# Kernel tuning notes

Measured on AMD Instinct MI355X. Metric: run time of the kernel, lower is better.

## Reference

```python
import jax, jax.numpy as jnp
import numpy as np

HEADS = 16  # module init arg `heads`


def setup_inputs() -> dict:
    key = jax.random.key(0)
    k1, k2, k3 = jax.random.split(key, 3)
    B, T, D = 2, 2048, 1024
    x = jax.random.normal(k1, (B, T, D), dtype=jnp.float32)
    w_qkv = jax.random.normal(k2, (D, 3 * D), dtype=jnp.float32) * (1.0 / np.sqrt(D))
    w_proj = jax.random.normal(k3, (D, D), dtype=jnp.float32) * (1.0 / np.sqrt(D))
    b_proj = jnp.zeros((D,), dtype=jnp.float32)
    return {"x": x, "w_qkv": w_qkv, "w_proj": w_proj, "b_proj": b_proj,
            "window": 16, "stride": 16}


def reference(x, w_qkv, w_proj, b_proj, window, stride):
    B, T, D = x.shape
    H = HEADS
    hd = D // H
    scale = 1.0 / np.sqrt(hd)

    qkv = x @ w_qkv                              # [B,T,3D]
    qkv = qkv.reshape(B, T, 3, H, hd)
    q = jnp.transpose(qkv[:, :, 0], (0, 2, 1, 3))  # [B,H,T,hd]
    k = jnp.transpose(qkv[:, :, 1], (0, 2, 1, 3))
    v = jnp.transpose(qkv[:, :, 2], (0, 2, 1, 3))

    # Local window attention: pad front with zeros (matches F.pad), gather
    # sliding windows so patches[..., t, w, :] = k_padded[..., t + w, :].
    pad = window - 1
    k_pad = jnp.pad(k, ((0, 0), (0, 0), (pad, 0), (0, 0)))
    v_pad = jnp.pad(v, ((0, 0), (0, 0), (pad, 0), (0, 0)))
    win_idx = jnp.arange(T)[:, None] + jnp.arange(window)[None, :]  # [T,W]
    pk = k_pad[:, :, win_idx]                    # [B,H,T,W,hd]
    pv = v_pad[:, :, win_idx]                    # [B,H,T,W,hd]

    attn_local = jnp.einsum('bhtd,bhtwd->bhtw', q, pk) * scale
    attn_local = jax.nn.softmax(attn_local, axis=-1)  # zero-pad keys included, as in torch
    out_local = jnp.einsum('bhtw,bhtwd->bhtd', attn_local, pv)

    # Strided global attention
    g_idx = jnp.arange(0, T, stride)
    kg = k[:, :, g_idx]                          # [B,H,G,hd]
    vg = v[:, :, g_idx]
    attn_g = jnp.einsum('bhtd,bhgd->bhtg', q, kg) * scale
    attn_g = jax.nn.softmax(attn_g, axis=-1)
    out_global = jnp.einsum('bhtg,bhgd->bhtd', attn_g, vg)

    out = out_local + out_global                 # [B,H,T,hd]
    out = jnp.transpose(out, (0, 2, 1, 3)).reshape(B, T, D)
    return out @ w_proj + b_proj
```

## Files before the change

kernel.cpp:

```cpp
#include <hip/hip_runtime.h>
#include <hip/hip_bf16.h>

#define BB 2
#define TT 2048
#define DD 1024
#define HH 16
#define HD 64
#define WIN 16
#define NG 128
#define QKVLD 3072
#define QB 128

typedef __bf16 bf16x8 __attribute__((ext_vector_type(8)));
typedef _Float16 f16x8 __attribute__((ext_vector_type(8)));
typedef float f32x4 __attribute__((ext_vector_type(4)));
typedef _Float16 h2 __attribute__((ext_vector_type(2)));
typedef __fp16 pk2_t __attribute__((ext_vector_type(2)));

__device__ __forceinline__ unsigned short f2bf(float f) {
    union { float f; unsigned int i; } x; x.f = f;
    unsigned int r = x.i + 0x7FFFu + ((x.i >> 16) & 1u);
    return (unsigned short)(r >> 16);
}
__device__ __forceinline__ unsigned short f2h(float f) {
    union { _Float16 h; unsigned short u; } x; x.h = (_Float16)f; return x.u;
}
__device__ __forceinline__ unsigned int pk2h(float lo, float hi) {
    union { pk2_t h; unsigned int u; } X;
    X.h = __builtin_amdgcn_cvt_pkrtz(lo, hi);
    return X.u;
}

__device__ __forceinline__ void gll16(const unsigned short* g, unsigned short* l) {
    __builtin_amdgcn_global_load_lds(
        (const __attribute__((address_space(1))) void*)g,
        (__attribute__((address_space(3))) void*)l,
        16, 0, 0);
}

__global__ __launch_bounds__(256) void prepass_kernel(
    const float* __restrict__ x,
    const float* __restrict__ w_qkv,
    const float* __restrict__ w_proj,
    unsigned short* __restrict__ xb,
    unsigned short* __restrict__ wqkvT,
    unsigned short* __restrict__ wprojT)
{
    __shared__ float tile[64][65];
    const int bid = blockIdx.x;
    const int tid = threadIdx.x;

    if (bid < 2048) {
        const size_t i = ((size_t)bid * 256 + tid) * 8;
        float4 f0 = *(const float4*)(x + i);
        float4 f1 = *(const float4*)(x + i + 4);
        ushort4 a = { f2bf(f0.x), f2bf(f0.y), f2bf(f0.z), f2bf(f0.w) };
        ushort4 b = { f2bf(f1.x), f2bf(f1.y), f2bf(f1.z), f2bf(f1.w) };
        *(ushort4*)(xb + i) = a;
        *(ushort4*)(xb + i + 4) = b;
        return;
    }

    const float* w;
    unsigned short* wT;
    int nblk, kblk, N;
    if (bid < 2816) {
        const int b2 = bid - 2048;
        w = w_qkv; wT = wqkvT; N = 3072;
        nblk = b2 % 48; kblk = b2 / 48;
    } else {
        const int b2 = bid - 2816;
        w = w_proj; wT = wprojT; N = 1024;
        nblk = b2 % 16; kblk = b2 / 16;
    }
    const int K = 1024;
    const int n0 = nblk * 64, k0 = kblk * 64;

    {
        const int krow = tid >> 2;
        const int nc0  = (tid & 3) * 16;
        const float* src = w + (size_t)(k0 + krow) * N + n0 + nc0;
        float4 f0 = *(const float4*)(src);
        float4 f1 = *(const float4*)(src + 4);
        float4 f2 = *(const float4*)(src + 8);
        float4 f3 = *(const float4*)(src + 12);
        *(float4*)&tile[krow][nc0]      = f0;
        *(float4*)&tile[krow][nc0 + 4]  = f1;
        *(float4*)&tile[krow][nc0 + 8]  = f2;
        *(float4*)&tile[krow][nc0 + 12] = f3;
    }
    __syncthreads();
    #pragma unroll
    for (int rep = 0; rep < 2; ++rep) {
        const int n   = (tid >> 3) + rep * 32;
        const int kc0 = (tid & 7) * 8;
        union { uint4 v; unsigned short u[8]; } o;
        #pragma unroll
        for (int j = 0; j < 8; ++j) o.u[j] = f2bf(tile[kc0 + j][n]);
        *(uint4*)(wT + (size_t)(n0 + n) * K + k0 + kc0) = o.v;
    }
}

template<int MODE, int TN>
__global__ __launch_bounds__(256) void gemm_kernel(
    const unsigned short* __restrict__ A,
    const unsigned short* __restrict__ Bt,
    void* __restrict__ Cp,
    const float* __restrict__ bias,
    int M, int N, int K)
{
    constexpr int NJ = TN / 32;
    constexpr int BRW = TN / 4;
    __shared__ __align__(16) unsigned short As[128 * 64];
    __shared__ __align__(16) unsigned short Bs[TN * 64];
    const int tid  = threadIdx.x;
    const int wave = tid >> 6;
    const int lane = tid & 63;
    const int lm   = lane & 15;
    const int quad = lane >> 4;
    const int wm   = (wave >> 1) * 64;
    const int wn   = (wave & 1) * (TN / 2);
    const int bm   = blockIdx.y * 128;
    const int bn   = blockIdx.x * TN;

    f32x4 acc[4][NJ];
    const f32x4 z4 = { 0.f, 0.f, 0.f, 0.f };
    #pragma unroll
    for (int i = 0; i < 4; ++i)
        #pragma unroll
        for (int j = 0; j < NJ; ++j) acc[i][j] = z4;

    const int lrow = lane >> 3;
    const int lcol = ((lane & 7) ^ lrow) * 8;
    const unsigned short* gA = A  + (size_t)(bm + wave * 32  + lrow) * K + lcol;
    const unsigned short* gB = Bt + (size_t)(bn + wave * BRW + lrow) * K + lcol;
    unsigned short* lA = &As[(wave * 32)  * 64];
    unsigned short* lB = &Bs[(wave * BRW) * 64];

    const int sx = lm & 7;
    for (int k0 = 0; k0 < K; k0 += 64) {
        __syncthreads();
        #pragma unroll
        for (int s = 0; s < 4; ++s)
            gll16(gA + k0 + (size_t)(8 * s) * K, lA + (8 * s) * 64);
        #pragma unroll
        for (int s = 0; s < BRW / 8; ++s)
            gll16(gB + k0 + (size_t)(8 * s) * K, lB + (8 * s) * 64);
        __syncthreads();
        #pragma unroll
        for (int kk = 0; kk < 2; ++kk) {
            bf16x8 af[4], bfr[NJ];
            #pragma unroll
            for (int i = 0; i < 4; ++i)
                af[i] = *(const bf16x8*)&As[(wm + i * 16 + lm) * 64
                                            + (((kk * 4 + quad) ^ sx) * 8)];
            #pragma unroll
            for (int j = 0; j < NJ; ++j)
                bfr[j] = *(const bf16x8*)&Bs[(wn + j * 16 + lm) * 64
                                             + (((kk * 4 + quad) ^ sx) * 8)];
            #pragma unroll
            for (int i = 0; i < 4; ++i)
                #pragma unroll
                for (int j = 0; j < NJ; ++j)
                    acc[i][j] = __builtin_amdgcn_mfma_f32_16x16x32_bf16(
                        af[i], bfr[j], acc[i][j], 0, 0, 0);
        }
    }

    #pragma unroll
    for (int i = 0; i < 4; ++i) {
        #pragma unroll
        for (int r = 0; r < 4; ++r) {
            const int row = bm + wm + i * 16 + quad * 4 + r;
            #pragma unroll
            for (int j = 0; j < NJ; ++j) {
                const int col = bn + wn + j * 16 + lm;
                float v = acc[i][j][r];
                if constexpr (MODE == 0) {
                    ((unsigned short*)Cp)[(size_t)row * N + col] = f2h(v);
                } else {
                    ((float*)Cp)[(size_t)row * N + col] = v + bias[col];
                }
            }
        }
    }
}

__device__ __forceinline__ f16x8 pfrag(unsigned int fa0, unsigned int fa1,
                                       unsigned int fb0, unsigned int fb1,
                                       int quad) {
    const unsigned int t16_0 = (quad == 2) ? fb0 : fa0;
    const unsigned int t16_1 = (quad == 2) ? fb1 : fa1;
    const unsigned int t32_0 = (quad == 0) ? fb0 : fa0;
    const unsigned int t32_1 = (quad == 0) ? fb1 : fa1;
    const unsigned int t48_0 = (quad == 1) ? fb0 : fa0;
    const unsigned int t48_1 = (quad == 1) ? fb1 : fa1;
    const unsigned int s16_0 = (unsigned int)__shfl_xor((int)t16_0, 16, 64);
    const unsigned int s16_1 = (unsigned int)__shfl_xor((int)t16_1, 16, 64);
    const unsigned int s32_0 = (unsigned int)__shfl_xor((int)t32_0, 32, 64);
    const unsigned int s32_1 = (unsigned int)__shfl_xor((int)t32_1, 32, 64);
    const unsigned int s48_0 = (unsigned int)__shfl_xor((int)t48_0, 48, 64);
    const unsigned int s48_1 = (unsigned int)__shfl_xor((int)t48_1, 48, 64);
    unsigned int w0, w1, w2, w3;
    if (quad == 0)      { w0 = fa0;   w1 = fa1;   w2 = s16_0; w3 = s16_1; }
    else if (quad == 1) { w0 = s48_0; w1 = s48_1; w2 = s32_0; w3 = s32_1; }
    else if (quad == 2) { w0 = s32_0; w1 = s32_1; w2 = s48_0; w3 = s48_1; }
    else                { w0 = s16_0; w1 = s16_1; w2 = fb0;   w3 = fb1;   }
    union { unsigned int u[4]; f16x8 v; } R;
    R.u[0] = w0; R.u[1] = w1; R.u[2] = w2; R.u[3] = w3;
    return R.v;
}

__global__ __launch_bounds__(512, 4) void attn_kernel(
    const unsigned short* __restrict__ qkv,
    unsigned short* __restrict__ attn_out)
{
    __shared__ __align__(16) unsigned short smem[19584];
    unsigned short* const Kg  = smem;
    unsigned short* const Kl  = smem + 9216;
    unsigned short* const VgT = smem;
    unsigned short* const VlT = smem + 9216;
    unsigned short* const Ep  = smem;

    const int tid  = threadIdx.x;
    const int wave = tid >> 6;
    const int lane = tid & 63;
    const int lm   = lane & 15;
    const int quad = lane >> 4;
    const int bx   = blockIdx.x;
    const int bh   = bx >> 4;
    const int t0   = (bx & 15) * QB;
    const int b    = bh >> 4;
    const int h    = bh & 15;

    const size_t baseQ = (size_t)(b * TT) * QKVLD + h * HD;

    const int r  = (tid & 255) >> 1;
    const int hf = tid & 1;
    uint4 va[4];
    if (tid < 256) {
        const unsigned short* ks = qkv + baseQ + 1024 + (size_t)(16 * r) * QKVLD + hf * 32;
        const unsigned short* vs = ks + 1024;
        unsigned short* kd = Kg + r * 72 + hf * 32;
        #pragma unroll
        for (int j = 0; j < 4; ++j) *(uint4*)(kd + j * 8) = *(const uint4*)(ks + j * 8);
        #pragma unroll
        for (int j = 0; j < 4; ++j) va[j] = *(const uint4*)(vs + j * 8);
    } else {
        const int tl = t0 - 15 + r;
        unsigned short* kld = Kl + r * 72 + hf * 32;
        if (tl < 0 || tl >= TT) {
            const uint4 z = { 0, 0, 0, 0 };
            #pragma unroll
            for (int j = 0; j < 4; ++j) { *(uint4*)(kld + j * 8) = z; va[j] = z; }
        } else {
            const unsigned short* kls = qkv + baseQ + 1024 + (size_t)tl * QKVLD + hf * 32;
            const unsigned short* vls = kls + 1024;
            #pragma unroll
            for (int j = 0; j < 4; ++j) *(uint4*)(kld + j * 8) = *(const uint4*)(kls + j * 8);
            #pragma unroll
            for (int j = 0; j < 4; ++j) va[j] = *(const uint4*)(vls + j * 8);
        }
    }
    if (tid < 32) {
        const int r2 = 128 + (tid >> 1);
        const int tl = t0 - 15 + r2;
        unsigned short* kld = Kl + r2 * 72 + hf * 32;
        if (tl < 0 || tl >= TT) {
            const uint4 z = { 0, 0, 0, 0 };
            #pragma unroll
            for (int j = 0; j < 4; ++j) *(uint4*)(kld + j * 8) = z;
        } else {
            const unsigned short* kls = qkv + baseQ + 1024 + (size_t)tl * QKVLD + hf * 32;
            #pragma unroll
            for (int j = 0; j < 4; ++j) *(uint4*)(kld + j * 8) = *(const uint4*)(kls + j * 8);
        }
    }

    f16x8 qf[2];
    {
        const unsigned short* qrow = qkv + baseQ + (size_t)(t0 + 16 * wave + lm) * QKVLD;
        const h2 sc = { (_Float16)0.125f, (_Float16)0.125f };
        #pragma unroll
        for (int c = 0; c < 2; ++c) {
            union { uint4 u; h2 hh[4]; f16x8 v; } U;
            U.u = *(const uint4*)(qrow + c * 32 + quad * 8);
            #pragma unroll
            for (int k = 0; k < 4; ++k) U.hh[k] *= sc;
            qf[c] = U.v;
        }
    }

    __syncthreads();

    f32x4 sg[8], sl[2];
    const f32x4 z4 = { 0.f, 0.f, 0.f, 0.f };
    #pragma unroll
    for (int f = 0; f < 8; ++f) sg[f] = z4;
    sl[0] = z4; sl[1] = z4;
    __builtin_amdgcn_s_setprio(1);
    #pragma unroll
    for (int f = 0; f < 8; ++f)
        #pragma unroll
        for (int c = 0; c < 2; ++c)
            sg[f] = __builtin_amdgcn_mfma_f32_16x16x32_f16(
                *(const f16x8*)&Kg[(16 * f + lm) * 72 + c * 32 + quad * 8], qf[c],
                sg[f], 0, 0, 0);
    #pragma unroll
    for (int f = 0; f < 2; ++f)
        #pragma unroll
        for (int c = 0; c < 2; ++c)
            sl[f] = __builtin_amdgcn_mfma_f32_16x16x32_f16(
                *(const f16x8*)&Kl[(16 * wave + 16 * f + lm) * 72 + c * 32 + quad * 8], qf[c],
                sl[f], 0, 0, 0);
    __builtin_amdgcn_s_setprio(0);

    float invg, invl;
    {
        float dg = 0.f, dl = 0.f;
        #pragma unroll
        for (int f = 0; f < 8; ++f)
            #pragma unroll
            for (int rr = 0; rr < 4; ++rr) {
                float e = __expf(sg[f][rr]); sg[f][rr] = e; dg += e;
            }
        #pragma unroll
        for (int f = 0; f < 2; ++f)
            #pragma unroll
            for (int rr = 0; rr < 4; ++rr) {
                const int j2 = 16 * f + quad * 4 + rr;
                const bool in = (j2 >= lm) && (j2 <= lm + 15);
                float e = in ? __expf(sl[f][rr]) : 0.f;
                sl[f][rr] = e; dl += e;
            }
        dg += __shfl_xor(dg, 16, 64);
        dg += __shfl_xor(dg, 32, 64);
        dl += __shfl_xor(dl, 16, 64);
        dl += __shfl_xor(dl, 32, 64);
        invg = 1.f / dg;
        invl = 1.f / dl;
    }

    f16x8 pa0, pa1, pa2, pa3, pal;
    {
        #pragma unroll
        for (int f = 0; f < 8; ++f)
            #pragma unroll
            for (int rr = 0; rr < 4; ++rr) sg[f][rr] *= invg;
        #pragma unroll
        for (int f = 0; f < 2; ++f)
            #pragma unroll
            for (int rr = 0; rr < 4; ++rr) sl[f][rr] *= invl;
        pa0 = pfrag(pk2h(sg[0][0], sg[0][1]), pk2h(sg[0][2], sg[0][3]),
                    pk2h(sg[1][0], sg[1][1]), pk2h(sg[1][2], sg[1][3]), quad);
        pa1 = pfrag(pk2h(sg[2][0], sg[2][1]), pk2h(sg[2][2], sg[2][3]),
                    pk2h(sg[3][0], sg[3][1]), pk2h(sg[3][2], sg[3][3]), quad);
        pa2 = pfrag(pk2h(sg[4][0], sg[4][1]), pk2h(sg[4][2], sg[4][3]),
                    pk2h(sg[5][0], sg[5][1]), pk2h(sg[5][2], sg[5][3]), quad);
        pa3 = pfrag(pk2h(sg[6][0], sg[6][1]), pk2h(sg[6][2], sg[6][3]),
                    pk2h(sg[7][0], sg[7][1]), pk2h(sg[7][2], sg[7][3]), quad);
        pal = pfrag(pk2h(sl[0][0], sl[0][1]), pk2h(sl[0][2], sl[0][3]),
                    pk2h(sl[1][0], sl[1][1]), pk2h(sl[1][2], sl[1][3]), quad);
    }

    __syncthreads();

    {
        union { uint4 u[4]; unsigned short s[32]; } U;
        #pragma unroll
        for (int j = 0; j < 4; ++j) U.u[j] = va[j];
        if (tid < 256) {
            #pragma unroll
            for (int j = 0; j < 32; ++j) VgT[(hf * 32 + j) * 136 + r] = U.s[j];
        } else {
            #pragma unroll
            for (int j = 0; j < 32; ++j) VlT[(hf * 32 + j) * 152 + r] = U.s[j];
        }
        if (tid < 32) {
            const int r2 = 128 + (tid >> 1);
            const int tl = t0 - 15 + r2;
            union { uint4 u[4]; unsigned short s[32]; } W;
            if (tl < 0 || tl >= TT) {
                const uint4 z = { 0, 0, 0, 0 };
                #pragma unroll
                for (int j = 0; j < 4; ++j) W.u[j] = z;
            } else {
                const unsigned short* vls = qkv + baseQ + 2048 + (size_t)tl * QKVLD + hf * 32;
                #pragma unroll
                for (int j = 0; j < 4; ++j) W.u[j] = *(const uint4*)(vls + j * 8);
            }
            #pragma unroll
            for (int j = 0; j < 32; ++j) VlT[(hf * 32 + j) * 152 + r2] = W.s[j];
        }
    }

    __syncthreads();

    f32x4 o[4];
    #pragma unroll
    for (int c = 0; c < 4; ++c) o[c] = z4;
    __builtin_amdgcn_s_setprio(1);
    #pragma unroll
    for (int c = 0; c < 4; ++c) {
        o[c] = __builtin_amdgcn_mfma_f32_16x16x32_f16(
            pa0, *(const f16x8*)&VgT[(16 * c + lm) * 136 + 0 * 32 + quad * 8], o[c], 0, 0, 0);
        o[c] = __builtin_amdgcn_mfma_f32_16x16x32_f16(
            pa1, *(const f16x8*)&VgT[(16 * c + lm) * 136 + 1 * 32 + quad * 8], o[c], 0, 0, 0);
        o[c] = __builtin_amdgcn_mfma_f32_16x16x32_f16(
            pa2, *(const f16x8*)&VgT[(16 * c + lm) * 136 + 2 * 32 + quad * 8], o[c], 0, 0, 0);
        o[c] = __builtin_amdgcn_mfma_f32_16x16x32_f16(
            pa3, *(const f16x8*)&VgT[(16 * c + lm) * 136 + 3 * 32 + quad * 8], o[c], 0, 0, 0);
        o[c] = __builtin_amdgcn_mfma_f32_16x16x32_f16(
            pal, *(const f16x8*)&VlT[(16 * c + lm) * 152 + 16 * wave + quad * 8], o[c], 0, 0, 0);
    }
    __builtin_amdgcn_s_setprio(0);

    __syncthreads();

    {
        unsigned short* const Pw = Ep + wave * (16 * 72);
        #pragma unroll
        for (int rr = 0; rr < 4; ++rr) {
            unsigned short* orow_p = Pw + (quad * 4 + rr) * 72;
            #pragma unroll
            for (int c = 0; c < 4; ++c) orow_p[16 * c + lm] = f2bf(o[c][rr]);
        }
        const int orow = lane >> 2;
        const int ocol = (lane & 3) * 16;
        const uint4 d0 = *(const uint4*)&Pw[orow * 72 + ocol];
        const uint4 d1 = *(const uint4*)&Pw[orow * 72 + ocol + 8];
        unsigned short* dst = attn_out + (size_t)(b * TT + t0 + 16 * wave + orow) * DD + h * HD + ocol;
        *(uint4*)(dst)     = d0;
        *(uint4*)(dst + 8) = d1;
    }
}

extern "C" void kernel_launch(void* const* d_in, const int* in_sizes, int n_in,
                              void* d_out, int out_size, void* d_ws, size_t ws_size,
                              hipStream_t stream) {
    const float* x      = (const float*)d_in[0];
    const float* w_qkv  = (const float*)d_in[1];
    const float* w_proj = (const float*)d_in[2];
    const float* b_proj = (const float*)d_in[3];

    char* ws = (char*)d_ws;
    unsigned short* qkv    = (unsigned short*)ws;
    unsigned short* xb     = (unsigned short*)(ws + 25165824);
    unsigned short* attnb  = xb;
    unsigned short* wqkvT  = (unsigned short*)(ws + 25165824 + 8388608);
    unsigned short* wprojT = (unsigned short*)(ws + 25165824 + 8388608 + 6291456);
    float* out = (float*)d_out;

    prepass_kernel<<<3072, 256, 0, stream>>>(x, w_qkv, w_proj, xb, wqkvT, wprojT);

    gemm_kernel<0, 128><<<dim3(3072 / 128, 4096 / 128), 256, 0, stream>>>(
        xb, wqkvT, qkv, nullptr, 4096, 3072, 1024);

    attn_kernel<<<dim3(BB * HH * (TT / QB)), 512, 0, stream>>>(qkv, attnb);

    gemm_kernel<1, 64><<<dim3(1024 / 64, 4096 / 128), 256, 0, stream>>>(
        attnb, wprojT, out, b_proj, 4096, 1024, 1024);
}
```

Measured before the change: 150.4 us.

## Add 256x192 double-buffered GEMM kernel for QKV projection

Replaces the 128x128-tile QKV GEMM with a new 512-thread kernel that uses 256x192 output tiles, a double-buffered K loop of 32 with global-to-LDS async loads, and XOR-swizzled LDS layout. Larger tiles raise arithmetic intensity and operand reuse per block, and the double buffering overlaps loads with MFMA work. The grid shrinks to 256 blocks, roughly one per CU, so tail effects and occupancy may limit the gain. The epilogue writes fp16 scalars without vectorization.

```diff
diff --git a/kernel.cpp b/kernel.cpp
--- a/kernel.cpp
+++ b/kernel.cpp
@@ -98,6 +98,83 @@
         #pragma unroll
         for (int j = 0; j < 8; ++j) o.u[j] = f2bf(tile[kc0 + j][n]);
         *(uint4*)(wT + (size_t)(n0 + n) * K + k0 + kc0) = o.v;
+    }
+}
+
+__global__ __launch_bounds__(512, 2) void gemm_big_kernel(
+    const unsigned short* __restrict__ A,
+    const unsigned short* __restrict__ Bt,
+    unsigned short* __restrict__ C)
+{
+    __shared__ __align__(16) unsigned short As[2][256 * 32];
+    __shared__ __align__(16) unsigned short Bs[2][192 * 32];
+    const int tid  = threadIdx.x;
+    const int wave = tid >> 6;
+    const int lane = tid & 63;
+    const int lm   = lane & 15;
+    const int quad = lane >> 4;
+    const int wm   = (wave >> 1) * 64;
+    const int wn   = (wave & 1) * 96;
+    const int bm   = blockIdx.y * 256;
+    const int bn   = blockIdx.x * 192;
+    const int K = 1024, N = 3072;
+
+    f32x4 acc[4][6];
+    const f32x4 z4 = { 0.f, 0.f, 0.f, 0.f };
+    #pragma unroll
+    for (int i = 0; i < 4; ++i)
+        #pragma unroll
+        for (int j = 0; j < 6; ++j) acc[i][j] = z4;
+
+    const int srow = lane >> 2;
+    const int schk = (lane & 3) ^ (srow & 3);
+    const unsigned short* gA0 = A  + (size_t)(bm + (2 * wave)     * 16 + srow) * K + schk * 8;
+    const unsigned short* gA1 = A  + (size_t)(bm + (2 * wave + 1) * 16 + srow) * K + schk * 8;
+    const unsigned short* gB0 = Bt + (size_t)(bn + wave * 16 + srow) * K + schk * 8;
+    const unsigned short* gB1 = Bt + (size_t)(bn + (8 + wave) * 16 + srow) * K + schk * 8;
+
+    auto stage = [&](int buf, int k0) {
+        gll16(gA0 + k0, &As[buf][(2 * wave)     * 512]);
+        gll16(gA1 + k0, &As[buf][(2 * wave + 1) * 512]);
+        gll16(gB0 + k0, &Bs[buf][wave * 512]);
+        if (wave < 4) gll16(gB1 + k0, &Bs[buf][(8 + wave) * 512]);
+    };
+
+    stage(0, 0);
+    __syncthreads();
+
+    const int sx = lm & 3;
+    int cur = 0;
+    for (int ks = 0; ks < 32; ++ks) {
+        if (ks < 31) stage(cur ^ 1, (ks + 1) * 32);
+        bf16x8 af[4], bfr[6];
+        #pragma unroll
+        for (int i = 0; i < 4; ++i)
+            af[i] = *(const bf16x8*)&As[cur][(wm + i * 16 + lm) * 32 + ((quad ^ sx) * 8)];
+        #pragma unroll
+        for (int j = 0; j < 6; ++j)
+            bfr[j] = *(const bf16x8*)&Bs[cur][(wn + j * 16 + lm) * 32 + ((quad ^ sx) * 8)];
+        #pragma unroll
+        for (int i = 0; i < 4; ++i)
+            #pragma unroll
+            for (int j = 0; j < 6; ++j)
+                acc[i][j] = __builtin_amdgcn_mfma_f32_16x16x32_bf16(
+                    af[i], bfr[j], acc[i][j], 0, 0, 0);
+        __syncthreads();
+        cur ^= 1;
+    }
+
+    #pragma unroll
+    for (int i = 0; i < 4; ++i) {
+        #pragma unroll
+        for (int r = 0; r < 4; ++r) {
+            const int row = bm + wm + i * 16 + quad * 4 + r;
+            #pragma unroll
+            for (int j = 0; j < 6; ++j) {
+                const int col = bn + wn + j * 16 + lm;
+                C[(size_t)row * N + col] = f2h(acc[i][j][r]);
+            }
+        }
     }
 }
 
@@ -453,8 +530,8 @@
 
     prepass_kernel<<<3072, 256, 0, stream>>>(x, w_qkv, w_proj, xb, wqkvT, wprojT);
 
-    gemm_kernel<0, 128><<<dim3(3072 / 128, 4096 / 128), 256, 0, stream>>>(
-        xb, wqkvT, qkv, nullptr, 4096, 3072, 1024);
+    gemm_big_kernel<<<dim3(3072 / 192, 4096 / 256), 512, 0, stream>>>(
+        xb, wqkvT, qkv);
 
     attn_kernel<<<dim3(BB * HH * (TT / QB)), 512, 0, stream>>>(qkv, attnb);
 
```

New measurement: 157.3 us. 4.6% more time.

## Double-buffer GEMM LDS tiles with BK=32 and async prefetch

Applied to the files above, without the earlier changes.

The GEMM main loop now keeps two shared-memory buffers with a K-step of 32 and issues the global-to-LDS loads for the next tile before computing on the current one. Explicit vmcnt waits and raw barriers replace the paired __syncthreads, and MFMA issue runs at raised wave priority. The aim is to hide global load latency behind matrix math, at the cost of twice as many loop iterations and barriers. The hard-coded vmcnt counts depend on exactly how many loads each stage issues.

```diff
diff --git a/kernel.cpp b/kernel.cpp
--- a/kernel.cpp
+++ b/kernel.cpp
@@ -109,10 +109,11 @@
     const float* __restrict__ bias,
     int M, int N, int K)
 {
-    constexpr int NJ = TN / 32;
+    constexpr int NJ  = TN / 32;
     constexpr int BRW = TN / 4;
-    __shared__ __align__(16) unsigned short As[128 * 64];
-    __shared__ __align__(16) unsigned short Bs[TN * 64];
+    constexpr int NB  = BRW / 16;
+    __shared__ __align__(16) unsigned short As[2][128 * 32];
+    __shared__ __align__(16) unsigned short Bs[2][TN * 32];
     const int tid  = threadIdx.x;
     const int wave = tid >> 6;
     const int lane = tid & 63;
@@ -130,41 +131,52 @@
         #pragma unroll
         for (int j = 0; j < NJ; ++j) acc[i][j] = z4;
 
-    const int lrow = lane >> 3;
-    const int lcol = ((lane & 7) ^ lrow) * 8;
-    const unsigned short* gA = A  + (size_t)(bm + wave * 32  + lrow) * K + lcol;
-    const unsigned short* gB = Bt + (size_t)(bn + wave * BRW + lrow) * K + lcol;
-    unsigned short* lA = &As[(wave * 32)  * 64];
-    unsigned short* lB = &Bs[(wave * BRW) * 64];
-
-    const int sx = lm & 7;
-    for (int k0 = 0; k0 < K; k0 += 64) {
-        __syncthreads();
-        #pragma unroll
-        for (int s = 0; s < 4; ++s)
-            gll16(gA + k0 + (size_t)(8 * s) * K, lA + (8 * s) * 64);
-        #pragma unroll
-        for (int s = 0; s < BRW / 8; ++s)
-            gll16(gB + k0 + (size_t)(8 * s) * K, lB + (8 * s) * 64);
-        __syncthreads();
-        #pragma unroll
-        for (int kk = 0; kk < 2; ++kk) {
-            bf16x8 af[4], bfr[NJ];
-            #pragma unroll
-            for (int i = 0; i < 4; ++i)
-                af[i] = *(const bf16x8*)&As[(wm + i * 16 + lm) * 64
-                                            + (((kk * 4 + quad) ^ sx) * 8)];
+    const int srow = lane >> 2;
+    const int schk = (lane & 3) ^ (srow & 3);
+    const unsigned short* gA0 = A  + (size_t)(bm + wave * 32  + srow) * K + schk * 8;
+    const unsigned short* gA1 = gA0 + (size_t)16 * K;
+    const unsigned short* gB0 = Bt + (size_t)(bn + wave * BRW + srow) * K + schk * 8;
+    const unsigned short* gB1 = gB0 + (size_t)16 * K;
+
+    auto stage = [&](int buf, int k0) {
+        gll16(gA0 + k0, &As[buf][(wave * 32) * 32]);
+        gll16(gA1 + k0, &As[buf][(wave * 32 + 16) * 32]);
+        gll16(gB0 + k0, &Bs[buf][(wave * BRW) * 32]);
+        if constexpr (NB == 2) gll16(gB1 + k0, &Bs[buf][(wave * BRW + 16) * 32]);
+    };
+
+    stage(0, 0);
+
+    const int sx = lm & 3;
+    int cur = 0;
+    for (int k0 = 0; k0 < K; k0 += 32) {
+        if (k0 + 32 < K) {
+            stage(cur ^ 1, k0 + 32);
+            if constexpr (NB == 2) asm volatile("s_waitcnt vmcnt(4)" ::: "memory");
+            else                   asm volatile("s_waitcnt vmcnt(3)" ::: "memory");
+        } else {
+            asm volatile("s_waitcnt vmcnt(0)" ::: "memory");
+        }
+        __builtin_amdgcn_s_barrier();
+        __builtin_amdgcn_sched_barrier(0);
+        bf16x8 af[4], bfr[NJ];
+        #pragma unroll
+        for (int i = 0; i < 4; ++i)
+            af[i] = *(const bf16x8*)&As[cur][(wm + i * 16 + lm) * 32 + ((quad ^ sx) * 8)];
+        #pragma unroll
+        for (int j = 0; j < NJ; ++j)
+            bfr[j] = *(const bf16x8*)&Bs[cur][(wn + j * 16 + lm) * 32 + ((quad ^ sx) * 8)];
+        __builtin_amdgcn_s_setprio(1);
+        #pragma unroll
+        for (int i = 0; i < 4; ++i)
             #pragma unroll
             for (int j = 0; j < NJ; ++j)
-                bfr[j] = *(const bf16x8*)&Bs[(wn + j * 16 + lm) * 64
-                                             + (((kk * 4 + quad) ^ sx) * 8)];
-            #pragma unroll
-            for (int i = 0; i < 4; ++i)
-                #pragma unroll
-                for (int j = 0; j < NJ; ++j)
-                    acc[i][j] = __builtin_amdgcn_mfma_f32_16x16x32_bf16(
-                        af[i], bfr[j], acc[i][j], 0, 0, 0);
-        }
+                acc[i][j] = __builtin_amdgcn_mfma_f32_16x16x32_bf16(
+                    af[i], bfr[j], acc[i][j], 0, 0, 0);
+        __builtin_amdgcn_s_setprio(0);
+        __builtin_amdgcn_sched_barrier(0);
+        __builtin_amdgcn_s_barrier();
+        cur ^= 1;
     }
 
     #pragma unroll
```

Result: slower. 156.1 us (+3.8%).
